# Kernel tuning notes

Hardware: AMD Instinct MI355X
Metric: run time of the kernel (lower is better)

## Reference

```python
import jax, jax.numpy as jnp
import numpy as np

GAMMA = 0.001

def softor(x, axis, gamma=GAMMA):
    # gamma * logsumexp(x/gamma); renormalize by global max if it exceeds 1 (NSFR convention)
    s = gamma * jax.nn.logsumexp(x / gamma, axis=axis)
    m = jnp.max(s)
    return jnp.where(m > 1.0, s / m, s)

def softand(x, axis, gamma=GAMMA):
    # soft conjunction: -gamma * logsumexp(-x/gamma) (soft-min), same renormalization
    s = -gamma * jax.nn.logsumexp(-x / gamma, axis=axis)
    m = jnp.max(s)
    return jnp.where(m > 1.0, s / m, s)

def clause_fn(x, I_c):
    # x: (B, G) valuations; I_c: (G, S, L) atom indices for one clause.
    # torch.gather(V_tild, 1, I_tild)[b,g,s,l] == x[b, I_c[g,s,l]] -> plain take.
    g = jnp.take(x, I_c, axis=1)        # (B, G, S, L)
    p = softand(g, axis=3)              # (B, G, S): conjunction over body literals
    return softor(p, axis=2)            # (B, G): disjunction over substitutions

def setup_inputs() -> dict:
    key = jax.random.key(0)
    k1, k2 = jax.random.split(key)
    C, B, G, S, L = 16, 64, 2048, 8, 4
    x = jax.random.uniform(k1, (B, G), dtype=jnp.float32)
    I = jax.random.randint(k2, (C, G, S, L), 0, G, dtype=jnp.int32)
    return {"x": x, "I": I, "infer_step": 3}

def reference(x, I, infer_step):
    C = I.shape[0]
    R = jnp.broadcast_to(x[None], (C,) + x.shape)   # (C, B, G)
    def step(R, _):
        # r(R): one ClauseFunction per clause, vmapped over the clause axis
        r_R = jax.vmap(clause_fn)(R, I)             # (C, B, G)
        # softor([R, r_R], dim=2): stack along a new axis at position 2, reduce it
        R_new = softor(jnp.stack([R, r_R], axis=2), axis=2)
        return R_new, None
    R, _ = jax.lax.scan(step, R, None, length=infer_step)
    return R
```

## Files before the change

kernel.cpp:

```cpp
#include <hip/hip_runtime.h>


namespace {
constexpr int C = 16, B = 64, G = 2048, S = 8, L = 4;
}

__device__ __forceinline__ float4 f4min(float4 a, float4 b) {
    return make_float4(fminf(a.x,b.x), fminf(a.y,b.y), fminf(a.z,b.z), fminf(a.w,b.w));
}
__device__ __forceinline__ float4 f4max(float4 a, float4 b) {
    return make_float4(fmaxf(a.x,b.x), fmaxf(a.y,b.y), fmaxf(a.z,b.z), fmaxf(a.w,b.w));
}

__global__ __launch_bounds__(256, 4) void k_step(const float* __restrict__ src, int step0,
                                                 const int* __restrict__ I,
                                                 float* __restrict__ R) {
    __shared__ float4 lds4[G];

    const int blk = blockIdx.x, tid = threadIdx.x;
    const int bchunk = blk & 7, gtile = (blk >> 3) & 7, c = blk >> 6;
    const int g = gtile * 256 + tid, b0 = bchunk * 8;

    const int4* Ib = (const int4*)(I + (size_t)(c * G + g) * (S * L));
    int4 ix[S];
#pragma unroll
    for (int s = 0; s < S; ++s) ix[s] = Ib[s];

    const int rbase = step0 ? b0 : (c * B + b0);

    float4 ca[4], cb[4];
#pragma unroll
    for (int j = 0; j < 4; ++j) {
        const float4* rp = (const float4*)(src + (size_t)(rbase + j) * G);
        ca[j] = rp[tid]; cb[j] = rp[tid + 256];
    }

#pragma unroll
    for (int grp = 0; grp < 2; ++grp) {
        __syncthreads();
        {
            int col0 = 4 * tid, col1 = 4 * (tid + 256);
            lds4[col0 + 0] = make_float4(ca[0].x, ca[1].x, ca[2].x, ca[3].x);
            lds4[col0 + 1] = make_float4(ca[0].y, ca[1].y, ca[2].y, ca[3].y);
            lds4[col0 + 2] = make_float4(ca[0].z, ca[1].z, ca[2].z, ca[3].z);
            lds4[col0 + 3] = make_float4(ca[0].w, ca[1].w, ca[2].w, ca[3].w);
            lds4[col1 + 0] = make_float4(cb[0].x, cb[1].x, cb[2].x, cb[3].x);
            lds4[col1 + 1] = make_float4(cb[0].y, cb[1].y, cb[2].y, cb[3].y);
            lds4[col1 + 2] = make_float4(cb[0].z, cb[1].z, cb[2].z, cb[3].z);
            lds4[col1 + 3] = make_float4(cb[0].w, cb[1].w, cb[2].w, cb[3].w);
        }
        if (grp == 0) {
#pragma unroll
            for (int j = 0; j < 4; ++j) {
                const float4* rp = (const float4*)(src + (size_t)(rbase + 4 + j) * G);
                ca[j] = rp[tid]; cb[j] = rp[tid + 256];
            }
        }
        __syncthreads();

        float4 qq = make_float4(-3.0e38f, -3.0e38f, -3.0e38f, -3.0e38f);
#pragma unroll
        for (int s = 0; s < S; ++s) {
            int4 iv = ix[s];
            float4 w0 = lds4[iv.x], w1 = lds4[iv.y], w2 = lds4[iv.z], w3 = lds4[iv.w];
            qq = f4max(qq, f4min(f4min(w0, w1), f4min(w2, w3)));
        }
        const float4 s3 = f4max(lds4[g], qq);
        R[(size_t)(c * B + b0 + grp * 4 + 0) * G + g] = s3.x;
        R[(size_t)(c * B + b0 + grp * 4 + 1) * G + g] = s3.y;
        R[(size_t)(c * B + b0 + grp * 4 + 2) * G + g] = s3.z;
        R[(size_t)(c * B + b0 + grp * 4 + 3) * G + g] = s3.w;
    }
}

extern "C" void kernel_launch(void* const* d_in, const int* in_sizes, int n_in,
                              void* d_out, int out_size, void* d_ws, size_t ws_size,
                              hipStream_t stream) {
    const float* x = (const float*)d_in[0];
    const int*   I = (const int*)d_in[1];
    float* out = (float*)d_out;
    float* Rw  = (float*)d_ws;

    k_step<<<C * 8 * 8, 256, 0, stream>>>(x,  1, I, Rw);
    k_step<<<C * 8 * 8, 256, 0, stream>>>(Rw, 0, I, Rw);
    k_step<<<C * 8 * 8, 256, 0, stream>>>(Rw, 0, I, out);
}
```

Baseline: 102.2 us.

## Fuse all inference steps into one kernel with LDS-resident row state

The three per-step launches are replaced by one kernel. Each 1024-thread block owns one clause and four batch rows across all of G, keeps those rows in LDS between steps, and writes to global memory only after the last step. This removes the workspace round trips, the repeated index reloads and two launches. In exchange the grid is only 256 blocks of one large block each, so occupancy and latency hiding are lower, and each thread holds two sets of indices in registers.

```diff
diff --git a/kernel.cpp b/kernel.cpp
--- a/kernel.cpp
+++ b/kernel.cpp
@@ -3,6 +3,7 @@
 
 namespace {
 constexpr int C = 16, B = 64, G = 2048, S = 8, L = 4;
+constexpr int STEPS = 3;
 }
 
 __device__ __forceinline__ float4 f4min(float4 a, float4 b) {
@@ -12,64 +13,61 @@
     return make_float4(fmaxf(a.x,b.x), fmaxf(a.y,b.y), fmaxf(a.z,b.z), fmaxf(a.w,b.w));
 }
 
-__global__ __launch_bounds__(256, 4) void k_step(const float* __restrict__ src, int step0,
-                                                 const int* __restrict__ I,
-                                                 float* __restrict__ R) {
+__global__ __launch_bounds__(1024) void k_all(const float* __restrict__ x,
+                                              const int* __restrict__ I,
+                                              float* __restrict__ out) {
     __shared__ float4 lds4[G];
 
-    const int blk = blockIdx.x, tid = threadIdx.x;
-    const int bchunk = blk & 7, gtile = (blk >> 3) & 7, c = blk >> 6;
-    const int g = gtile * 256 + tid, b0 = bchunk * 8;
+    const int tid = threadIdx.x;
+    const int bq = blockIdx.x & 15, c = blockIdx.x >> 4;
+    const int b0 = bq * 4;
+    const int ga = tid, gb = tid + 1024;
 
-    const int4* Ib = (const int4*)(I + (size_t)(c * G + g) * (S * L));
-    int4 ix[S];
+    const int4* Ipa = (const int4*)(I + (size_t)(c * G + ga) * (S * L));
+    const int4* Ipb = (const int4*)(I + (size_t)(c * G + gb) * (S * L));
+    int4 ixa[S], ixb[S];
 #pragma unroll
-    for (int s = 0; s < S; ++s) ix[s] = Ib[s];
+    for (int s = 0; s < S; ++s) { ixa[s] = Ipa[s]; ixb[s] = Ipb[s]; }
 
-    const int rbase = step0 ? b0 : (c * B + b0);
-
-    float4 ca[4], cb[4];
+    float2 pr[4];
 #pragma unroll
-    for (int j = 0; j < 4; ++j) {
-        const float4* rp = (const float4*)(src + (size_t)(rbase + j) * G);
-        ca[j] = rp[tid]; cb[j] = rp[tid + 256];
-    }
+    for (int j = 0; j < 4; ++j)
+        pr[j] = ((const float2*)(x + (size_t)(b0 + j) * G))[tid];
+    lds4[2 * tid]     = make_float4(pr[0].x, pr[1].x, pr[2].x, pr[3].x);
+    lds4[2 * tid + 1] = make_float4(pr[0].y, pr[1].y, pr[2].y, pr[3].y);
+    __syncthreads();
 
 #pragma unroll
-    for (int grp = 0; grp < 2; ++grp) {
-        __syncthreads();
-        {
-            int col0 = 4 * tid, col1 = 4 * (tid + 256);
-            lds4[col0 + 0] = make_float4(ca[0].x, ca[1].x, ca[2].x, ca[3].x);
-            lds4[col0 + 1] = make_float4(ca[0].y, ca[1].y, ca[2].y, ca[3].y);
-            lds4[col0 + 2] = make_float4(ca[0].z, ca[1].z, ca[2].z, ca[3].z);
-            lds4[col0 + 3] = make_float4(ca[0].w, ca[1].w, ca[2].w, ca[3].w);
-            lds4[col1 + 0] = make_float4(cb[0].x, cb[1].x, cb[2].x, cb[3].x);
-            lds4[col1 + 1] = make_float4(cb[0].y, cb[1].y, cb[2].y, cb[3].y);
-            lds4[col1 + 2] = make_float4(cb[0].z, cb[1].z, cb[2].z, cb[3].z);
-            lds4[col1 + 3] = make_float4(cb[0].w, cb[1].w, cb[2].w, cb[3].w);
-        }
-        if (grp == 0) {
-#pragma unroll
-            for (int j = 0; j < 4; ++j) {
-                const float4* rp = (const float4*)(src + (size_t)(rbase + 4 + j) * G);
-                ca[j] = rp[tid]; cb[j] = rp[tid + 256];
-            }
-        }
-        __syncthreads();
-
-        float4 qq = make_float4(-3.0e38f, -3.0e38f, -3.0e38f, -3.0e38f);
+    for (int step = 0; step < STEPS; ++step) {
+        float4 qa = make_float4(-3.0e38f, -3.0e38f, -3.0e38f, -3.0e38f);
+        float4 qb = qa;
 #pragma unroll
         for (int s = 0; s < S; ++s) {
-            int4 iv = ix[s];
-            float4 w0 = lds4[iv.x], w1 = lds4[iv.y], w2 = lds4[iv.z], w3 = lds4[iv.w];
-            qq = f4max(qq, f4min(f4min(w0, w1), f4min(w2, w3)));
+            int4 iv = ixa[s];
+            qa = f4max(qa, f4min(f4min(lds4[iv.x], lds4[iv.y]),
+                                 f4min(lds4[iv.z], lds4[iv.w])));
+            iv = ixb[s];
+            qb = f4max(qb, f4min(f4min(lds4[iv.x], lds4[iv.y]),
+                                 f4min(lds4[iv.z], lds4[iv.w])));
         }
-        const float4 s3 = f4max(lds4[g], qq);
-        R[(size_t)(c * B + b0 + grp * 4 + 0) * G + g] = s3.x;
-        R[(size_t)(c * B + b0 + grp * 4 + 1) * G + g] = s3.y;
-        R[(size_t)(c * B + b0 + grp * 4 + 2) * G + g] = s3.z;
-        R[(size_t)(c * B + b0 + grp * 4 + 3) * G + g] = s3.w;
+        const float4 sa = f4max(lds4[ga], qa);
+        const float4 sb = f4max(lds4[gb], qb);
+
+        if (step < STEPS - 1) {
+            __syncthreads();
+            lds4[ga] = sa;
+            lds4[gb] = sb;
+            __syncthreads();
+        } else {
+            out[(size_t)(c * B + b0 + 0) * G + ga] = sa.x;
+            out[(size_t)(c * B + b0 + 1) * G + ga] = sa.y;
+            out[(size_t)(c * B + b0 + 2) * G + ga] = sa.z;
+            out[(size_t)(c * B + b0 + 3) * G + ga] = sa.w;
+            out[(size_t)(c * B + b0 + 0) * G + gb] = sb.x;
+            out[(size_t)(c * B + b0 + 1) * G + gb] = sb.y;
+            out[(size_t)(c * B + b0 + 2) * G + gb] = sb.z;
+            out[(size_t)(c * B + b0 + 3) * G + gb] = sb.w;
+        }
     }
 }
 
@@ -79,9 +77,6 @@
     const float* x = (const float*)d_in[0];
     const int*   I = (const int*)d_in[1];
     float* out = (float*)d_out;
-    float* Rw  = (float*)d_ws;
 
-    k_step<<<C * 8 * 8, 256, 0, stream>>>(x,  1, I, Rw);
-    k_step<<<C * 8 * 8, 256, 0, stream>>>(Rw, 0, I, Rw);
-    k_step<<<C * 8 * 8, 256, 0, stream>>>(Rw, 0, I, out);
+    k_all<<<C * 16, 1024, 0, stream>>>(x, I, out);
 }
```

New measurement: 97.88 us. 1.04x faster.
